# Optimization experiments

Hardware: AMD Instinct MI355X
Metric: run time of the kernel (lower is better)

## Reference

```python
import jax, jax.numpy as jnp
import numpy as np

N_NODES = 100000
N_EDGES = 1600000
DIMS = [256, 128, 64, 32, 16]  # halving pyramid from number_of_x=256 down to number_of_classes=16
N_LAYERS = len(DIMS) - 1


def setup_inputs() -> dict:
    key = jax.random.key(0)
    ks = jax.random.split(key, 3 + N_LAYERS)
    inp = {
        "x": jax.random.normal(ks[0], (N_NODES, DIMS[0]), jnp.float32),
        "src": jax.random.randint(ks[1], (N_EDGES,), 0, N_NODES),
        "dst": jax.random.randint(ks[2], (N_EDGES,), 0, N_NODES),
    }
    for i in range(N_LAYERS):
        inp[f"W{i}"] = jax.random.normal(ks[3 + i], (DIMS[i], DIMS[i + 1]), jnp.float32) / np.sqrt(DIMS[i])
        inp[f"b{i}"] = jnp.zeros((DIMS[i + 1],), jnp.float32)   # GraphConv bias
        inp[f"sb{i}"] = jnp.zeros((1,), jnp.float32)            # module's extra scalar bias
    return inp


def _gcn_layer(h, src, dst, W, b, norm_src, norm_dst):
    # DGL GraphConv, norm='both', in_feats >= out_feats -> transform first, then aggregate
    h = h * norm_src[:, None]                                    # D_out^{-1/2} * X
    h = h @ W                                                    # GEMM
    agg = jax.ops.segment_sum(h[src], dst, num_segments=N_NODES) # SpMM aggregation
    return agg * norm_dst[:, None] + b                           # D_in^{-1/2}, + bias


def reference(x, src, dst, W0, b0, sb0, W1, b1, sb1, W2, b2, sb2, W3, b3, sb3):
    ones = jnp.ones((N_EDGES,), jnp.float32)
    out_deg = jax.ops.segment_sum(ones, src, num_segments=N_NODES)
    in_deg = jax.ops.segment_sum(ones, dst, num_segments=N_NODES)
    norm_src = jnp.maximum(out_deg, 1.0) ** -0.5
    norm_dst = jnp.maximum(in_deg, 1.0) ** -0.5
    h = x
    for W, b, sb in ((W0, b0, sb0), (W1, b1, sb1), (W2, b2, sb2), (W3, b3, sb3)):
        h = jax.nn.relu(_gcn_layer(h, src, dst, W, b, norm_src, norm_dst) + sb)
    return jax.nn.softmax(h, axis=1)
```

## Files before the change

kernel.cpp:

```cpp
#include <hip/hip_runtime.h>
#include <hip/hip_bf16.h>

#define N_NODES 100000
#define N_EDGES 1600000
#define NRANGE 16
#define NSLICE 32
#define RSZ (N_NODES / NRANGE)
#define ESL (N_EDGES / NSLICE)
#define EQ (ESL / 4)

typedef unsigned short u16;
typedef unsigned int u32;

static __device__ __forceinline__ u16 f2bf(float f) {
    union { float f; u32 u; } v; v.f = f;
    u32 u = v.u;
    u += 0x7FFFu + ((u >> 16) & 1u);
    return (u16)(u >> 16);
}
static __device__ __forceinline__ float bflo(u32 w) {
    union { u32 u; float f; } v; v.u = w << 16; return v.f;
}
static __device__ __forceinline__ float bfhi(u32 w) {
    union { u32 u; float f; } v; v.u = w & 0xFFFF0000u; return v.f;
}

__global__ __launch_bounds__(256) void hist_kernel(
    const int* __restrict__ src, const int* __restrict__ dst,
    u32* __restrict__ dslice, u32* __restrict__ sslice) {
    __shared__ u32 db[RSZ];
    __shared__ u32 sb[RSZ];
    const int t = threadIdx.x;
    const int r = blockIdx.x & (NRANGE - 1);
    const int s = blockIdx.x >> 4;
    const u32 r0 = (u32)r * RSZ;
    for (int i = t; i < RSZ; i += 256) { db[i] = 0u; sb[i] = 0u; }
    __syncthreads();
    const int e0 = s * ESL;
    for (int k = t; k < EQ; k += 256) {
        int idx = e0 + k * 4;
        uint4 d4 = *reinterpret_cast<const uint4*>(&dst[idx]);
        uint4 s4 = *reinterpret_cast<const uint4*>(&src[idx]);
        u32 li;
        li = d4.x - r0; if (li < RSZ) atomicAdd(&db[li], 1u);
        li = d4.y - r0; if (li < RSZ) atomicAdd(&db[li], 1u);
        li = d4.z - r0; if (li < RSZ) atomicAdd(&db[li], 1u);
        li = d4.w - r0; if (li < RSZ) atomicAdd(&db[li], 1u);
        li = s4.x - r0; if (li < RSZ) atomicAdd(&sb[li], 1u);
        li = s4.y - r0; if (li < RSZ) atomicAdd(&sb[li], 1u);
        li = s4.z - r0; if (li < RSZ) atomicAdd(&sb[li], 1u);
        li = s4.w - r0; if (li < RSZ) atomicAdd(&sb[li], 1u);
    }
    __syncthreads();
    u32* dbase = dslice + (size_t)(r * NSLICE + s) * RSZ;
    u32* sbase = sslice + (size_t)(r * NSLICE + s) * RSZ;
    for (int i = t; i < RSZ; i += 256) { dbase[i] = db[i]; sbase[i] = sb[i]; }
}

__global__ __launch_bounds__(256) void prep_kernel(
    u32* __restrict__ dslice, const u32* __restrict__ sslice,
    u32* __restrict__ indeg, float* __restrict__ norm_src, float* __restrict__ norm_dst) {
    int n = blockIdx.x * 256 + threadIdx.x;
    if (n >= N_NODES) return;
    int r = n / RSZ;
    int i = n - r * RSZ;
    size_t base = (size_t)(r * NSLICE) * RSZ + i;
    u32 accd = 0u, accs = 0u;
#pragma unroll
    for (int s = 0; s < NSLICE; ++s) {
        u32 c = dslice[base + (size_t)s * RSZ];
        dslice[base + (size_t)s * RSZ] = accd;
        accd += c;
        accs += sslice[base + (size_t)s * RSZ];
    }
    indeg[n] = accd;
    norm_dst[n] = rsqrtf((float)(accd < 1u ? 1u : accd));
    norm_src[n] = rsqrtf((float)(accs < 1u ? 1u : accs));
}

#define SCAN_B 512
#define SCAN_NBLK ((N_NODES + SCAN_B - 1) / SCAN_B)

__global__ __launch_bounds__(SCAN_B) void scan1_kernel(
    const u32* __restrict__ indeg, u32* __restrict__ row_ptr, u32* __restrict__ bsum) {
    __shared__ u32 s[SCAN_B];
    int t = threadIdx.x;
    int gid = blockIdx.x * SCAN_B + t;
    u32 v = (gid < N_NODES) ? indeg[gid] : 0u;
    s[t] = v;
    __syncthreads();
    for (int off = 1; off < SCAN_B; off <<= 1) {
        u32 x = (t >= off) ? s[t - off] : 0u;
        __syncthreads();
        s[t] += x;
        __syncthreads();
    }
    if (gid < N_NODES) row_ptr[gid + 1] = s[t];
    if (t == SCAN_B - 1) bsum[blockIdx.x] = s[t];
}

__global__ __launch_bounds__(256) void scan2_kernel(u32* __restrict__ bsum, u32* __restrict__ boff) {
    __shared__ u32 s[256];
    int t = threadIdx.x;
    s[t] = (t < SCAN_NBLK) ? bsum[t] : 0u;
    __syncthreads();
    for (int off = 1; off < 256; off <<= 1) {
        u32 x = (t >= off) ? s[t - off] : 0u;
        __syncthreads();
        s[t] += x;
        __syncthreads();
    }
    if (t < SCAN_NBLK) boff[t] = (t == 0) ? 0u : s[t - 1];
}

__global__ __launch_bounds__(256) void scan3_kernel(u32* __restrict__ row_ptr, const u32* __restrict__ boff) {
    int gid = blockIdx.x * 256 + threadIdx.x;
    if (gid < N_NODES) {
        row_ptr[gid + 1] += boff[gid / SCAN_B];
        if (gid == 0) row_ptr[0] = 0u;
    }
}

__global__ __launch_bounds__(256) void fill2_kernel(
    const int* __restrict__ src, const int* __restrict__ dst,
    const u32* __restrict__ row_ptr, const u32* __restrict__ dslice,
    u32* __restrict__ col) {
    __shared__ u32 cur[RSZ];
    const int t = threadIdx.x;
    const int r = blockIdx.x & (NRANGE - 1);
    const int s = blockIdx.x >> 4;
    const u32 r0 = (u32)r * RSZ;
    const u32* dbase = dslice + (size_t)(r * NSLICE + s) * RSZ;
    for (int i = t; i < RSZ; i += 256) cur[i] = 0u;
    __syncthreads();
    const int e0 = s * ESL;
    for (int k = t; k < EQ; k += 256) {
        int idx = e0 + k * 4;
        uint4 d4 = *reinterpret_cast<const uint4*>(&dst[idx]);
        uint4 s4 = *reinterpret_cast<const uint4*>(&src[idx]);
        u32 li, rk;
        li = d4.x - r0; if (li < RSZ) { rk = atomicAdd(&cur[li], 1u); col[row_ptr[d4.x] + dbase[li] + rk] = s4.x; }
        li = d4.y - r0; if (li < RSZ) { rk = atomicAdd(&cur[li], 1u); col[row_ptr[d4.y] + dbase[li] + rk] = s4.y; }
        li = d4.z - r0; if (li < RSZ) { rk = atomicAdd(&cur[li], 1u); col[row_ptr[d4.z] + dbase[li] + rk] = s4.z; }
        li = d4.w - r0; if (li < RSZ) { rk = atomicAdd(&cur[li], 1u); col[row_ptr[d4.w] + dbase[li] + rk] = s4.w; }
    }
}

template <int DIN, int DOUT>
__global__ __launch_bounds__(256) void gemm_kernel(
    const float* __restrict__ h, const float* __restrict__ W,
    const float* __restrict__ norm_src, u16* __restrict__ T) {
    constexpr int TM = 64;
    constexpr int KT = 32;
    constexpr int JBLKS = DOUT / 4;
    constexpr int NPT = (TM * DOUT) / (256 * 4);

    __shared__ float hs[KT][TM + 4];
    __shared__ float ws[KT][DOUT];

    const int t = threadIdx.x;
    const int m0 = blockIdx.x * TM;
    const int jblk = t % JBLKS;
    const int nblk = t / JBLKS;
    const int n0 = nblk * NPT;

    float acc[NPT][4];
    for (int i = 0; i < NPT; ++i)
        for (int j = 0; j < 4; ++j) acc[i][j] = 0.f;

    for (int k0 = 0; k0 < DIN; k0 += KT) {
        for (int it = 0; it < 2; ++it) {
            int f = t + it * 256;
            int row = f / (KT / 4);
            int c4  = f % (KT / 4);
            float4 v = make_float4(0.f, 0.f, 0.f, 0.f);
            int gr = m0 + row;
            if (gr < N_NODES)
                v = *reinterpret_cast<const float4*>(&h[gr * DIN + k0 + c4 * 4]);
            hs[c4 * 4 + 0][row] = v.x;
            hs[c4 * 4 + 1][row] = v.y;
            hs[c4 * 4 + 2][row] = v.z;
            hs[c4 * 4 + 3][row] = v.w;
        }
        constexpr int WQ = KT * DOUT / 4;
        constexpr int WITERS = (WQ + 255) / 256;
        for (int it = 0; it < WITERS; ++it) {
            int f = t + it * 256;
            if (f < WQ) {
                int row = f / JBLKS;
                int c4  = f % JBLKS;
                *reinterpret_cast<float4*>(&ws[row][c4 * 4]) =
                    *reinterpret_cast<const float4*>(&W[(k0 + row) * DOUT + c4 * 4]);
            }
        }
        __syncthreads();

#pragma unroll 4
        for (int k = 0; k < KT; ++k) {
            float4 wv = *reinterpret_cast<const float4*>(&ws[k][jblk * 4]);
            float a[NPT];
            if constexpr (NPT % 4 == 0) {
#pragma unroll
                for (int i = 0; i < NPT; i += 4)
                    *reinterpret_cast<float4*>(&a[i]) =
                        *reinterpret_cast<const float4*>(&hs[k][n0 + i]);
            } else if constexpr (NPT == 2) {
                *reinterpret_cast<float2*>(&a[0]) =
                    *reinterpret_cast<const float2*>(&hs[k][n0]);
            } else {
                a[0] = hs[k][n0];
            }
#pragma unroll
            for (int i = 0; i < NPT; ++i) {
                acc[i][0] = fmaf(a[i], wv.x, acc[i][0]);
                acc[i][1] = fmaf(a[i], wv.y, acc[i][1]);
                acc[i][2] = fmaf(a[i], wv.z, acc[i][2]);
                acc[i][3] = fmaf(a[i], wv.w, acc[i][3]);
            }
        }
        __syncthreads();
    }

#pragma unroll
    for (int i = 0; i < NPT; ++i) {
        int n = m0 + n0 + i;
        if (n < N_NODES) {
            float s = norm_src[n];
            ushort4 o;
            o.x = f2bf(acc[i][0] * s);
            o.y = f2bf(acc[i][1] * s);
            o.z = f2bf(acc[i][2] * s);
            o.w = f2bf(acc[i][3] * s);
            *reinterpret_cast<ushort4*>(&T[n * DOUT + jblk * 4]) = o;
        }
    }
}

template <int D>
__global__ __launch_bounds__(256) void pull_kernel(
    const u16* __restrict__ T, const u32* __restrict__ row_ptr,
    const u32* __restrict__ col, const float* __restrict__ norm_dst,
    const float* __restrict__ b, const float* __restrict__ sb,
    float* __restrict__ h) {
    constexpr int TPN = D / 8;
    int tid = blockIdx.x * 256 + threadIdx.x;
    int n = tid / TPN;
    int c = (tid % TPN) * 8;
    if (n >= N_NODES) return;

    u32 beg = row_ptr[n], end = row_ptr[n + 1];
    float a[8];
#pragma unroll
    for (int j = 0; j < 8; ++j) a[j] = 0.f;

    u32 e = beg;
    for (; e + 1 < end; e += 2) {
        u32 s0 = col[e], s1 = col[e + 1];
        uint4 q0 = *reinterpret_cast<const uint4*>(&T[s0 * D + c]);
        uint4 q1 = *reinterpret_cast<const uint4*>(&T[s1 * D + c]);
        a[0] += bflo(q0.x) + bflo(q1.x);
        a[1] += bfhi(q0.x) + bfhi(q1.x);
        a[2] += bflo(q0.y) + bflo(q1.y);
        a[3] += bfhi(q0.y) + bfhi(q1.y);
        a[4] += bflo(q0.z) + bflo(q1.z);
        a[5] += bfhi(q0.z) + bfhi(q1.z);
        a[6] += bflo(q0.w) + bflo(q1.w);
        a[7] += bfhi(q0.w) + bfhi(q1.w);
    }
    if (e < end) {
        uint4 q0 = *reinterpret_cast<const uint4*>(&T[col[e] * D + c]);
        a[0] += bflo(q0.x); a[1] += bfhi(q0.x);
        a[2] += bflo(q0.y); a[3] += bfhi(q0.y);
        a[4] += bflo(q0.z); a[5] += bfhi(q0.z);
        a[6] += bflo(q0.w); a[7] += bfhi(q0.w);
    }

    float nd = norm_dst[n];
    float sv = sb[0];
    float4 b0 = *reinterpret_cast<const float4*>(&b[c]);
    float4 b1 = *reinterpret_cast<const float4*>(&b[c + 4]);
    float4 o0, o1;
    o0.x = fmaxf(a[0] * nd + b0.x + sv, 0.f);
    o0.y = fmaxf(a[1] * nd + b0.y + sv, 0.f);
    o0.z = fmaxf(a[2] * nd + b0.z + sv, 0.f);
    o0.w = fmaxf(a[3] * nd + b0.w + sv, 0.f);
    o1.x = fmaxf(a[4] * nd + b1.x + sv, 0.f);
    o1.y = fmaxf(a[5] * nd + b1.y + sv, 0.f);
    o1.z = fmaxf(a[6] * nd + b1.z + sv, 0.f);
    o1.w = fmaxf(a[7] * nd + b1.w + sv, 0.f);
    *reinterpret_cast<float4*>(&h[n * D + c])     = o0;
    *reinterpret_cast<float4*>(&h[n * D + c + 4]) = o1;
}

__global__ __launch_bounds__(256) void pull16_sm_kernel(
    const u16* __restrict__ T, const u32* __restrict__ row_ptr,
    const u32* __restrict__ col, const float* __restrict__ norm_dst,
    const float* __restrict__ b, const float* __restrict__ sb,
    float* __restrict__ out) {
    int tid = blockIdx.x * 256 + threadIdx.x;
    int n = tid >> 1;
    int c = (tid & 1) * 8;
    if (n >= N_NODES) return;

    u32 beg = row_ptr[n], end = row_ptr[n + 1];
    float a[8];
#pragma unroll
    for (int j = 0; j < 8; ++j) a[j] = 0.f;

    u32 e = beg;
    for (; e + 1 < end; e += 2) {
        u32 s0 = col[e], s1 = col[e + 1];
        uint4 q0 = *reinterpret_cast<const uint4*>(&T[s0 * 16 + c]);
        uint4 q1 = *reinterpret_cast<const uint4*>(&T[s1 * 16 + c]);
        a[0] += bflo(q0.x) + bflo(q1.x);
        a[1] += bfhi(q0.x) + bfhi(q1.x);
        a[2] += bflo(q0.y) + bflo(q1.y);
        a[3] += bfhi(q0.y) + bfhi(q1.y);
        a[4] += bflo(q0.z) + bflo(q1.z);
        a[5] += bfhi(q0.z) + bfhi(q1.z);
        a[6] += bflo(q0.w) + bflo(q1.w);
        a[7] += bfhi(q0.w) + bfhi(q1.w);
    }
    if (e < end) {
        uint4 q0 = *reinterpret_cast<const uint4*>(&T[col[e] * 16 + c]);
        a[0] += bflo(q0.x); a[1] += bfhi(q0.x);
        a[2] += bflo(q0.y); a[3] += bfhi(q0.y);
        a[4] += bflo(q0.z); a[5] += bfhi(q0.z);
        a[6] += bflo(q0.w); a[7] += bfhi(q0.w);
    }

    float nd = norm_dst[n];
    float sv = sb[0];
    float4 b0 = *reinterpret_cast<const float4*>(&b[c]);
    float4 b1 = *reinterpret_cast<const float4*>(&b[c + 4]);
    float o[8];
    o[0] = fmaxf(a[0] * nd + b0.x + sv, 0.f);
    o[1] = fmaxf(a[1] * nd + b0.y + sv, 0.f);
    o[2] = fmaxf(a[2] * nd + b0.z + sv, 0.f);
    o[3] = fmaxf(a[3] * nd + b0.w + sv, 0.f);
    o[4] = fmaxf(a[4] * nd + b1.x + sv, 0.f);
    o[5] = fmaxf(a[5] * nd + b1.y + sv, 0.f);
    o[6] = fmaxf(a[6] * nd + b1.z + sv, 0.f);
    o[7] = fmaxf(a[7] * nd + b1.w + sv, 0.f);

    float m = o[0];
#pragma unroll
    for (int j = 1; j < 8; ++j) m = fmaxf(m, o[j]);
    m = fmaxf(m, __shfl_xor(m, 1));
    float s = 0.f;
#pragma unroll
    for (int j = 0; j < 8; ++j) { o[j] = __expf(o[j] - m); s += o[j]; }
    s += __shfl_xor(s, 1);
    float inv = 1.f / s;
    float4 w0 = make_float4(o[0] * inv, o[1] * inv, o[2] * inv, o[3] * inv);
    float4 w1 = make_float4(o[4] * inv, o[5] * inv, o[6] * inv, o[7] * inv);
    *reinterpret_cast<float4*>(&out[n * 16 + c])     = w0;
    *reinterpret_cast<float4*>(&out[n * 16 + c + 4]) = w1;
}

extern "C" void kernel_launch(void* const* d_in, const int* in_sizes, int n_in,
                              void* d_out, int out_size, void* d_ws, size_t ws_size,
                              hipStream_t stream) {
    const float* x   = (const float*)d_in[0];
    const int*   src = (const int*)d_in[1];
    const int*   dst = (const int*)d_in[2];
    const float* W0 = (const float*)d_in[3];
    const float* b0 = (const float*)d_in[4];
    const float* sb0 = (const float*)d_in[5];
    const float* W1 = (const float*)d_in[6];
    const float* b1 = (const float*)d_in[7];
    const float* sb1 = (const float*)d_in[8];
    const float* W2 = (const float*)d_in[9];
    const float* b2 = (const float*)d_in[10];
    const float* sb2 = (const float*)d_in[11];
    const float* W3 = (const float*)d_in[12];
    const float* b3 = (const float*)d_in[13];
    const float* sb3 = (const float*)d_in[14];

    char* ws = (char*)d_ws;
    float* h        = (float*)ws;
    u16*   T        = (u16*)(ws + 51200000);
    u32*   dslice   = (u32*)(ws + 51200000);
    u32*   sslice   = (u32*)(ws + 64000000);
    u32*   col      = (u32*)(ws + 76800000);
    u32*   row_ptr  = (u32*)(ws + 83200000);
    float* norm_src = (float*)(ws + 83600016);
    float* norm_dst = (float*)(ws + 84000016);
    u32*   bsum     = (u32*)(ws + 84400016);
    u32*   boff     = (u32*)(ws + 84404016);
    u32*   indeg    = (u32*)(ws + 84408016);

    const int NB = (N_NODES + 255) / 256;
    const int MT = (N_NODES + 63) / 64;

    hist_kernel<<<NRANGE * NSLICE, 256, 0, stream>>>(src, dst, dslice, sslice);
    prep_kernel<<<NB, 256, 0, stream>>>(dslice, sslice, indeg, norm_src, norm_dst);
    scan1_kernel<<<SCAN_NBLK, SCAN_B, 0, stream>>>(indeg, row_ptr, bsum);
    scan2_kernel<<<1, 256, 0, stream>>>(bsum, boff);
    scan3_kernel<<<NB, 256, 0, stream>>>(row_ptr, boff);
    fill2_kernel<<<NRANGE * NSLICE, 256, 0, stream>>>(src, dst, row_ptr, dslice, col);

    gemm_kernel<256, 128><<<MT, 256, 0, stream>>>(x, W0, norm_src, T);
    pull_kernel<128><<<(N_NODES * 16 + 255) / 256, 256, 0, stream>>>(T, row_ptr, col, norm_dst, b0, sb0, h);

    gemm_kernel<128, 64><<<MT, 256, 0, stream>>>(h, W1, norm_src, T);
    pull_kernel<64><<<(N_NODES * 8 + 255) / 256, 256, 0, stream>>>(T, row_ptr, col, norm_dst, b1, sb1, h);

    gemm_kernel<64, 32><<<MT, 256, 0, stream>>>(h, W2, norm_src, T);
    pull_kernel<32><<<(N_NODES * 4 + 255) / 256, 256, 0, stream>>>(T, row_ptr, col, norm_dst, b2, sb2, h);

    gemm_kernel<32, 16><<<MT, 256, 0, stream>>>(h, W3, norm_src, T);
    pull16_sm_kernel<<<(N_NODES * 2 + 255) / 256, 256, 0, stream>>>(T, row_ptr, col, norm_dst, b3, sb3, (float*)d_out);
}
```

Baseline: 572.8 us.

## Replace FP32 SIMT GEMM with bf16 MFMA GEMM using pretransposed weights

Swaps the shared-memory FP32 FMA GEMM for a matrix-core kernel built on mfma_f32_16x16x32_bf16. Activations are converted to bf16 in registers and weights are pre-transposed into bf16 by a new prep kernel. The GEMMs are meant to stop being compute-bound on scalar FMAs. In exchange the products lose precision through bf16 inputs, and the output stores become scattered 2-byte writes.

After: 528.8 us. 1.08x faster.

```diff
diff --git a/kernel.cpp b/kernel.cpp
--- a/kernel.cpp
+++ b/kernel.cpp
@@ -12,6 +12,9 @@
 typedef unsigned short u16;
 typedef unsigned int u32;
 
+typedef float f32x4 __attribute__((ext_vector_type(4)));
+typedef short bf16x8 __attribute__((ext_vector_type(8)));
+
 static __device__ __forceinline__ u16 f2bf(float f) {
     union { float f; u32 u; } v; v.f = f;
     u32 u = v.u;
@@ -23,6 +26,11 @@
 }
 static __device__ __forceinline__ float bfhi(u32 w) {
     union { u32 u; float f; } v; v.u = w & 0xFFFF0000u; return v.f;
+}
+static __device__ __forceinline__ u32 cvtpk(float lo, float hi) {
+    u32 r;
+    asm("v_cvt_pk_bf16_f32 %0, %1, %2" : "=v"(r) : "v"(lo), "v"(hi));
+    return r;
 }
 
 __global__ __launch_bounds__(256) void hist_kernel(
@@ -146,92 +154,77 @@
     }
 }
 
+__global__ __launch_bounds__(256) void wtprep_kernel(
+    const float* __restrict__ W0, const float* __restrict__ W1,
+    const float* __restrict__ W2, const float* __restrict__ W3,
+    u16* __restrict__ wt) {
+    int i = blockIdx.x * 256 + threadIdx.x;
+    if (i >= 43520) return;
+    const float* W; int DIN, DOUT, local;
+    if (i < 32768)      { W = W0; DIN = 256; DOUT = 128; local = i; }
+    else if (i < 40960) { W = W1; DIN = 128; DOUT = 64;  local = i - 32768; }
+    else if (i < 43008) { W = W2; DIN = 64;  DOUT = 32;  local = i - 40960; }
+    else                { W = W3; DIN = 32;  DOUT = 16;  local = i - 43008; }
+    int j = local / DIN;
+    int k = local - j * DIN;
+    wt[i] = f2bf(W[k * DOUT + j]);
+}
+
 template <int DIN, int DOUT>
-__global__ __launch_bounds__(256) void gemm_kernel(
-    const float* __restrict__ h, const float* __restrict__ W,
+__global__ __launch_bounds__(256) void mgemm_kernel(
+    const float* __restrict__ h, const u16* __restrict__ Wt,
     const float* __restrict__ norm_src, u16* __restrict__ T) {
-    constexpr int TM = 64;
-    constexpr int KT = 32;
-    constexpr int JBLKS = DOUT / 4;
-    constexpr int NPT = (TM * DOUT) / (256 * 4);
-
-    __shared__ float hs[KT][TM + 4];
-    __shared__ float ws[KT][DOUT];
-
+    constexpr int NT = DOUT / 16;
+    constexpr int KS = DIN / 32;
     const int t = threadIdx.x;
-    const int m0 = blockIdx.x * TM;
-    const int jblk = t % JBLKS;
-    const int nblk = t / JBLKS;
-    const int n0 = nblk * NPT;
-
-    float acc[NPT][4];
-    for (int i = 0; i < NPT; ++i)
-        for (int j = 0; j < 4; ++j) acc[i][j] = 0.f;
-
-    for (int k0 = 0; k0 < DIN; k0 += KT) {
-        for (int it = 0; it < 2; ++it) {
-            int f = t + it * 256;
-            int row = f / (KT / 4);
-            int c4  = f % (KT / 4);
-            float4 v = make_float4(0.f, 0.f, 0.f, 0.f);
-            int gr = m0 + row;
-            if (gr < N_NODES)
-                v = *reinterpret_cast<const float4*>(&h[gr * DIN + k0 + c4 * 4]);
-            hs[c4 * 4 + 0][row] = v.x;
-            hs[c4 * 4 + 1][row] = v.y;
-            hs[c4 * 4 + 2][row] = v.z;
-            hs[c4 * 4 + 3][row] = v.w;
+    const int w = t >> 6;
+    const int l = t & 63;
+    const int lg = l >> 4;
+    const int lr = l & 15;
+    const int m0 = blockIdx.x * 128 + w * 32;
+
+    const int ra0 = min(m0 + lr, N_NODES - 1);
+    const int ra1 = min(m0 + 16 + lr, N_NODES - 1);
+
+    f32x4 acc[2][NT];
+#pragma unroll
+    for (int m = 0; m < 2; ++m)
+#pragma unroll
+        for (int nt = 0; nt < NT; ++nt) acc[m][nt] = (f32x4){0.f, 0.f, 0.f, 0.f};
+
+#pragma unroll
+    for (int ks = 0; ks < KS; ++ks) {
+        const int k0 = ks * 32 + lg * 8;
+        float4 a0 = *reinterpret_cast<const float4*>(&h[(size_t)ra0 * DIN + k0]);
+        float4 a1 = *reinterpret_cast<const float4*>(&h[(size_t)ra0 * DIN + k0 + 4]);
+        float4 b0 = *reinterpret_cast<const float4*>(&h[(size_t)ra1 * DIN + k0]);
+        float4 b1 = *reinterpret_cast<const float4*>(&h[(size_t)ra1 * DIN + k0 + 4]);
+        union { u32 u[4]; bf16x8 v; } af0, af1;
+        af0.u[0] = cvtpk(a0.x, a0.y); af0.u[1] = cvtpk(a0.z, a0.w);
+        af0.u[2] = cvtpk(a1.x, a1.y); af0.u[3] = cvtpk(a1.z, a1.w);
+        af1.u[0] = cvtpk(b0.x, b0.y); af1.u[1] = cvtpk(b0.z, b0.w);
+        af1.u[2] = cvtpk(b1.x, b1.y); af1.u[3] = cvtpk(b1.z, b1.w);
+#pragma unroll
+        for (int nt = 0; nt < NT; ++nt) {
+            union { uint4 q; bf16x8 v; } bf;
+            bf.q = *reinterpret_cast<const uint4*>(&Wt[(size_t)(nt * 16 + lr) * DIN + k0]);
+            acc[0][nt] = __builtin_amdgcn_mfma_f32_16x16x32_bf16(af0.v, bf.v, acc[0][nt], 0, 0, 0);
+            acc[1][nt] = __builtin_amdgcn_mfma_f32_16x16x32_bf16(af1.v, bf.v, acc[1][nt], 0, 0, 0);
         }
-        constexpr int WQ = KT * DOUT / 4;
-        constexpr int WITERS = (WQ + 255) / 256;
-        for (int it = 0; it < WITERS; ++it) {
-            int f = t + it * 256;
-            if (f < WQ) {
-                int row = f / JBLKS;
-                int c4  = f % JBLKS;
-                *reinterpret_cast<float4*>(&ws[row][c4 * 4]) =
-                    *reinterpret_cast<const float4*>(&W[(k0 + row) * DOUT + c4 * 4]);
+    }
+
+#pragma unroll
+    for (int m = 0; m < 2; ++m) {
+        const int rbase = m0 + m * 16 + lg * 4;
+#pragma unroll
+        for (int r = 0; r < 4; ++r) {
+            int row = rbase + r;
+            if (row < N_NODES) {
+                float ns = norm_src[row];
+#pragma unroll
+                for (int nt = 0; nt < NT; ++nt)
+                    T[(size_t)row * DOUT + nt * 16 + lr] = f2bf(acc[m][nt][r] * ns);
             }
-        }
-        __syncthreads();
-
-#pragma unroll 4
-        for (int k = 0; k < KT; ++k) {
-            float4 wv = *reinterpret_cast<const float4*>(&ws[k][jblk * 4]);
-            float a[NPT];
-            if constexpr (NPT % 4 == 0) {
-#pragma unroll
-                for (int i = 0; i < NPT; i += 4)
-                    *reinterpret_cast<float4*>(&a[i]) =
-                        *reinterpret_cast<const float4*>(&hs[k][n0 + i]);
-            } else if constexpr (NPT == 2) {
-                *reinterpret_cast<float2*>(&a[0]) =
-                    *reinterpret_cast<const float2*>(&hs[k][n0]);
-            } else {
-                a[0] = hs[k][n0];
-            }
-#pragma unroll
-            for (int i = 0; i < NPT; ++i) {
-                acc[i][0] = fmaf(a[i], wv.x, acc[i][0]);
-                acc[i][1] = fmaf(a[i], wv.y, acc[i][1]);
-                acc[i][2] = fmaf(a[i], wv.z, acc[i][2]);
-                acc[i][3] = fmaf(a[i], wv.w, acc[i][3]);
-            }
-        }
-        __syncthreads();
-    }
-
-#pragma unroll
-    for (int i = 0; i < NPT; ++i) {
-        int n = m0 + n0 + i;
-        if (n < N_NODES) {
-            float s = norm_src[n];
-            ushort4 o;
-            o.x = f2bf(acc[i][0] * s);
-            o.y = f2bf(acc[i][1] * s);
-            o.z = f2bf(acc[i][2] * s);
-            o.w = f2bf(acc[i][3] * s);
-            *reinterpret_cast<ushort4*>(&T[n * DOUT + jblk * 4]) = o;
         }
     }
 }
@@ -389,10 +382,12 @@
     u32*   bsum     = (u32*)(ws + 84400016);
     u32*   boff     = (u32*)(ws + 84404016);
     u32*   indeg    = (u32*)(ws + 84408016);
+    u16*   wt       = (u16*)(ws + 84808016);
 
     const int NB = (N_NODES + 255) / 256;
-    const int MT = (N_NODES + 63) / 64;
-
+    const int MT2 = (N_NODES + 127) / 128;
+
+    wtprep_kernel<<<170, 256, 0, stream>>>(W0, W1, W2, W3, wt);
     hist_kernel<<<NRANGE * NSLICE, 256, 0, stream>>>(src, dst, dslice, sslice);
     prep_kernel<<<NB, 256, 0, stream>>>(dslice, sslice, indeg, norm_src, norm_dst);
     scan1_kernel<<<SCAN_NBLK, SCAN_B, 0, stream>>>(indeg, row_ptr, bsum);
@@ -400,15 +395,15 @@
     scan3_kernel<<<NB, 256, 0, stream>>>(row_ptr, boff);
     fill2_kernel<<<NRANGE * NSLICE, 256, 0, stream>>>(src, dst, row_ptr, dslice, col);
 
-    gemm_kernel<256, 128><<<MT, 256, 0, stream>>>(x, W0, norm_src, T);
+    mgemm_kernel<256, 128><<<MT2, 256, 0, stream>>>(x, wt, norm_src, T);
     pull_kernel<128><<<(N_NODES * 16 + 255) / 256, 256, 0, stream>>>(T, row_ptr, col, norm_dst, b0, sb0, h);
 
-    gemm_kernel<128, 64><<<MT, 256, 0, stream>>>(h, W1, norm_src, T);
+    mgemm_kernel<128, 64><<<MT2, 256, 0, stream>>>(h, wt + 32768, norm_src, T);
     pull_kernel<64><<<(N_NODES * 8 + 255) / 256, 256, 0, stream>>>(T, row_ptr, col, norm_dst, b1, sb1, h);
 
-    gemm_kernel<64, 32><<<MT, 256, 0, stream>>>(h, W2, norm_src, T);
+    mgemm_kernel<64, 32><<<MT2, 256, 0, stream>>>(h, wt + 40960, norm_src, T);
     pull_kernel<32><<<(N_NODES * 4 + 255) / 256, 256, 0, stream>>>(T, row_ptr, col, norm_dst, b2, sb2, h);
 
-    gemm_kernel<32, 16><<<MT, 256, 0, stream>>>(h, W3, norm_src, T);
+    mgemm_kernel<32, 16><<<MT2, 256, 0, stream>>>(h, wt + 43008, norm_src, T);
     pull16_sm_kernel<<<(N_NODES * 2 + 255) / 256, 256, 0, stream>>>(T, row_ptr, col, norm_dst, b3, sb3, (float*)d_out);
 }
```
